# Performance work log

Hardware: AMD Instinct MI355X
Metric: run time of the kernel (lower is better)

The kernel has to match this reference:

```python
import jax, jax.numpy as jnp
import numpy as np

N_EMBD = 1024
HEAD_SIZE = N_EMBD  # source bug: Block passes n_embd as head_size
EPS = 1e-5

def layernorm(x, g, b):
    mu = jnp.mean(x, axis=-1, keepdims=True)
    var = jnp.var(x, axis=-1, keepdims=True)
    return (x - mu) * jax.lax.rsqrt(var + EPS) * g + b

def setup_inputs() -> dict:
    key = jax.random.key(0)
    ks = jax.random.split(key, 8)
    B, T, C = 4, 2048, N_EMBD
    s = lambda fan_in: 1.0 / np.sqrt(fan_in)
    return {
        "x": jax.random.normal(ks[0], (B, T, C), dtype=jnp.float32),
        "Wk": jax.random.uniform(ks[1], (C, HEAD_SIZE), jnp.float32, -s(C), s(C)),
        "Wq": jax.random.uniform(ks[2], (C, HEAD_SIZE), jnp.float32, -s(C), s(C)),
        "Wv": jax.random.uniform(ks[3], (C, HEAD_SIZE), jnp.float32, -s(C), s(C)),
        "W1": jax.random.uniform(ks[4], (C, 4 * C), jnp.float32, -s(C), s(C)),
        "b1": jnp.zeros((4 * C,), jnp.float32),
        "W2": jax.random.uniform(ks[5], (4 * C, C), jnp.float32, -s(4 * C), s(4 * C)),
        "b2": jnp.zeros((C,), jnp.float32),
        "g1": jnp.ones((C,), jnp.float32),
        "be1": jnp.zeros((C,), jnp.float32),
        "g2": jnp.ones((C,), jnp.float32),
        "be2": jnp.zeros((C,), jnp.float32),
    }

def reference(x, Wk, Wq, Wv, W1, b1, W2, b2, g1, be1, g2, be2):
    B, T, C = x.shape
    h = layernorm(x, g1, be1)
    q = h @ Wq              # [B,T,H]
    k = h @ Wk
    v = h @ Wv
    wei = jnp.einsum('bth,bsh->bts', q, k) / jnp.sqrt(jnp.float32(C))
    causal = jnp.tril(jnp.ones((T, T), dtype=bool))
    wei = jnp.where(causal, wei, -jnp.inf)
    wei = jax.nn.softmax(wei, axis=-1)
    sa = jnp.einsum('bts,bsh->bth', wei, v)
    x = x + sa
    h2 = layernorm(x, g2, be2)
    ff = jax.nn.relu(h2 @ W1 + b1) @ W2 + b2
    return x + ff
```

## Files before the change

kernel.cpp:

```cpp
#include <hip/hip_runtime.h>
#include <hip/hip_bf16.h>


typedef __bf16 bf16x8_t __attribute__((ext_vector_type(8)));
typedef float f32x4_t __attribute__((ext_vector_type(4)));

__device__ __forceinline__ unsigned short f2bf(float f) {
    unsigned int u = __float_as_uint(f);
    u += 0x7fffu + ((u >> 16) & 1u);
    return (unsigned short)(u >> 16);
}
__device__ __forceinline__ float bf2f(unsigned short u) {
    return __uint_as_float((unsigned int)u << 16);
}

__device__ __forceinline__ void gload16(const void* g, void* lds) {
    __builtin_amdgcn_global_load_lds(
        (const __attribute__((address_space(1))) unsigned int*)g,
        (__attribute__((address_space(3))) unsigned int*)lds, 16, 0, 0);
}

#define SB0() __builtin_amdgcn_sched_barrier(0)
#define BAR_LGKM() asm volatile("s_barrier\ns_waitcnt lgkmcnt(0)" ::: "memory")
#define BAR() asm volatile("s_barrier" ::: "memory")
#define VM4_BAR() asm volatile("s_waitcnt vmcnt(4)\ns_barrier" ::: "memory")
#define VM0_BAR() asm volatile("s_waitcnt vmcnt(0)\ns_barrier" ::: "memory")

enum { EPI_F32 = 0, EPI_BF16 = 1, EPI_BIAS_RELU_BF16 = 2, EPI_RESID_F32 = 3,
       EPI_BIAS_RESID_F32 = 4 };

template <int EPI, bool CSKIP, bool KLIM>
__global__ __launch_bounds__(512, 2) void gemm256(
    const unsigned short* __restrict__ A,
    const unsigned short* __restrict__ Bm,
    void* __restrict__ Cout,
    const float* __restrict__ bias,
    const float* __restrict__ resid,
    int M, int N, int K, int lda, int ldb, float scale,
    long long batA, long long batB, long long batC, long long batR)
{
    __shared__ __align__(16) unsigned char lds[131072];

    const int gx = gridDim.x;
    const int nwg = gx * gridDim.y;
    int bl = blockIdx.y * gx + blockIdx.x;
    bl = (bl & 7) * (nwg >> 3) + (bl >> 3);
    const int bx = bl % gx, by = bl / gx;

    const int row0 = by * 256, col0 = bx * 256;
    if (CSKIP && col0 > row0) return;

    const int bz = blockIdx.z;
    const unsigned short* Ab = A + (long long)bz * batA + (long long)row0 * lda;
    const unsigned short* Bb = Bm + (long long)bz * batB + (long long)col0 * ldb;

    const int tid = threadIdx.x, lane = tid & 63, wid = tid >> 6;
    const int wrM = (wid >> 2) * 128;
    const int wcN = (wid & 3) * 64;
    const int lr = lane & 15, lg = lane >> 4;

    int Keff = K;
    if (KLIM) { int kl = row0 + 256; Keff = kl < K ? kl : K; }
    const int nkt = Keff >> 6;

    const int c0 = wid * 128 + lane;
    const int crow = c0 >> 2;
    const int sg = (c0 & 3) ^ ((c0 >> 3) & 3);
    const unsigned short* gA0 = Ab + (long long)crow * lda + sg * 8;
    const unsigned short* gA1 = gA0 + 16ll * lda;
    const unsigned short* gB0 = Bb + (long long)crow * ldb + sg * 8;
    const unsigned short* gB1 = gB0 + 16ll * ldb;

    const int sw = (lg ^ ((lr >> 1) & 3)) << 4;
    const int aoff = (wrM + lr) * 64 + sw;
    const int boff = 16384 + (wcN + lr) * 64 + sw;

    f32x4_t acc[8][4];
#pragma unroll
    for (int m = 0; m < 8; ++m)
#pragma unroll
        for (int n = 0; n < 4; ++n)
            acc[m][n] = (f32x4_t){0.f, 0.f, 0.f, 0.f};

    auto stageR = [&](int b, int r, int ktn) {
        const int kk = r >> 1, op = r & 1;
        const int ke = ktn * 64 + kk * 32;
        unsigned char* d = lds + b * 65536 + kk * 32768 + op * 16384 + wid * 2048;
        const unsigned short* g0 = (op ? gB0 : gA0) + ke;
        const unsigned short* g1 = (op ? gB1 : gA1) + ke;
        gload16(g0, d);
        gload16(g1, d + 1024);
    };

    bf16x8_t af[4], bv[4];
    auto dsA4 = [&](int b, int kk, int mq) {
        const unsigned char* u = lds + b * 65536 + kk * 32768;
#pragma unroll
        for (int j = 0; j < 4; ++j)
            af[j] = *(const bf16x8_t*)(u + aoff + (mq * 4 + j) * 1024);
    };
    auto dsB4 = [&](int b, int kk) {
        const unsigned char* u = lds + b * 65536 + kk * 32768;
#pragma unroll
        for (int n = 0; n < 4; ++n)
            bv[n] = *(const bf16x8_t*)(u + boff + n * 1024);
    };
    auto mf16 = [&](int mq) {
        __builtin_amdgcn_s_setprio(1);
#pragma unroll
        for (int j = 0; j < 4; ++j)
#pragma unroll
            for (int n = 0; n < 4; ++n)
                acc[mq * 4 + j][n] = __builtin_amdgcn_mfma_f32_16x16x32_bf16(
                    af[j], bv[n], acc[mq * 4 + j][n], 0, 0, 0);
        __builtin_amdgcn_s_setprio(0);
    };

    stageR(0, 0, 0); stageR(0, 1, 0); stageR(0, 2, 0); stageR(0, 3, 0);
    VM4_BAR();

    int kt = 0;
    for (; kt < nkt - 1; ++kt) {
        const int buf = kt & 1, nb = buf ^ 1;
        dsA4(buf, 0, 0); dsB4(buf, 0);
        stageR(nb, 0, kt + 1);
        BAR_LGKM(); SB0();
        mf16(0); SB0();
        BAR();
        dsA4(buf, 0, 1);
        stageR(nb, 1, kt + 1);
        BAR_LGKM(); SB0();
        mf16(1); SB0();
        VM4_BAR();
        dsA4(buf, 1, 0); dsB4(buf, 1);
        stageR(nb, 2, kt + 1);
        BAR_LGKM(); SB0();
        mf16(0); SB0();
        BAR();
        dsA4(buf, 1, 1);
        stageR(nb, 3, kt + 1);
        BAR_LGKM(); SB0();
        mf16(1); SB0();
        VM4_BAR();
    }
    {
        const int buf = kt & 1;
        dsA4(buf, 0, 0); dsB4(buf, 0);
        BAR_LGKM(); SB0();
        mf16(0); SB0();
        BAR();
        dsA4(buf, 0, 1);
        BAR_LGKM(); SB0();
        mf16(1); SB0();
        VM0_BAR();
        dsA4(buf, 1, 0); dsB4(buf, 1);
        BAR_LGKM(); SB0();
        mf16(0); SB0();
        BAR();
        dsA4(buf, 1, 1);
        BAR_LGKM(); SB0();
        mf16(1); SB0();
    }

    const int ldc = N;
    float* Cf = (float*)Cout + (long long)bz * batC;
    unsigned short* Cb = (unsigned short*)Cout + (long long)bz * batC;
    const float* R = nullptr;
    if constexpr (EPI == EPI_RESID_F32 || EPI == EPI_BIAS_RESID_F32)
        R = resid + (long long)bz * batR;

#pragma unroll
    for (int m = 0; m < 8; ++m)
#pragma unroll
        for (int n = 0; n < 4; ++n)
#pragma unroll
            for (int j = 0; j < 4; ++j) {
                const int row = row0 + wrM + m * 16 + lg * 4 + j;
                const int col = col0 + wcN + n * 16 + lr;
                const long long idx = (long long)row * ldc + col;
                float v = acc[m][n][j] * scale;
                if constexpr (EPI == EPI_F32) {
                    Cf[idx] = v;
                } else if constexpr (EPI == EPI_BF16) {
                    Cb[idx] = f2bf(v);
                } else if constexpr (EPI == EPI_BIAS_RELU_BF16) {
                    v += bias[col];
                    v = v > 0.f ? v : 0.f;
                    Cb[idx] = f2bf(v);
                } else if constexpr (EPI == EPI_RESID_F32) {
                    Cf[idx] = v + R[idx];
                } else {
                    Cf[idx] = v + bias[col] + R[idx];
                }
            }
}

template <int EPI, bool CSKIP, bool KLIM>
__global__ __launch_bounds__(256, 2) void gemm128(
    const unsigned short* __restrict__ A,
    const unsigned short* __restrict__ Bm,
    void* __restrict__ Cout,
    const float* __restrict__ bias,
    const float* __restrict__ resid,
    int M, int N, int K, int lda, int ldb, float scale,
    long long batA, long long batB, long long batC, long long batR)
{
    __shared__ __align__(16) unsigned char lds[65536];

    const int gx = gridDim.x;
    const int nwg = gx * gridDim.y;
    int bl = blockIdx.y * gx + blockIdx.x;
    bl = (bl & 7) * (nwg >> 3) + (bl >> 3);
    const int bx = bl % gx, by = bl / gx;

    const int row0 = by * 128, col0 = bx * 128;
    if (CSKIP && col0 > row0) return;

    const int bz = blockIdx.z;
    const unsigned short* Ab = A + (long long)bz * batA + (long long)row0 * lda;
    const unsigned short* Bb = Bm + (long long)bz * batB + (long long)col0 * ldb;

    const int tid = threadIdx.x, lane = tid & 63, wid = tid >> 6;
    const int wrM = (wid >> 1) * 64;
    const int wcN = (wid & 1) * 64;
    const int lr = lane & 15, lg = lane >> 4;

    int Keff = K;
    if (KLIM) { int kl = row0 + 128; Keff = kl < K ? kl : K; }
    const int nkt = Keff >> 6;

    const int c0 = wid * 128 + lane;
    const int crow = c0 >> 2;
    const int sg = (c0 & 3) ^ ((c0 >> 3) & 3);
    const unsigned short* gA0 = Ab + (long long)crow * lda + sg * 8;
    const unsigned short* gA1 = gA0 + 16ll * lda;
    const unsigned short* gB0 = Bb + (long long)crow * ldb + sg * 8;
    const unsigned short* gB1 = gB0 + 16ll * ldb;

    const int sw = (lg ^ ((lr >> 1) & 3)) << 4;
    const int aoff = (wrM + lr) * 64 + sw;
    const int boff = 8192 + (wcN + lr) * 64 + sw;

    f32x4_t acc[4][4];
#pragma unroll
    for (int m = 0; m < 4; ++m)
#pragma unroll
        for (int n = 0; n < 4; ++n)
            acc[m][n] = (f32x4_t){0.f, 0.f, 0.f, 0.f};

    auto stage2 = [&](int b, int kk, int ktn) {
        const int ke = ktn * 64 + kk * 32;
        unsigned char* uA = lds + b * 32768 + kk * 16384 + wid * 2048;
        unsigned char* uB = uA + 8192;
        gload16(gA0 + ke, uA);
        gload16(gA1 + ke, uA + 1024);
        gload16(gB0 + ke, uB);
        gload16(gB1 + ke, uB + 1024);
    };

    bf16x8_t af[4], bv[4];
    auto dsAB = [&](int b, int kk) {
        const unsigned char* u = lds + b * 32768 + kk * 16384;
#pragma unroll
        for (int m = 0; m < 4; ++m)
            af[m] = *(const bf16x8_t*)(u + aoff + m * 1024);
#pragma unroll
        for (int n = 0; n < 4; ++n)
            bv[n] = *(const bf16x8_t*)(u + boff + n * 1024);
    };
    auto mf16 = [&]() {
        __builtin_amdgcn_s_setprio(1);
#pragma unroll
        for (int m = 0; m < 4; ++m)
#pragma unroll
            for (int n = 0; n < 4; ++n)
                acc[m][n] = __builtin_amdgcn_mfma_f32_16x16x32_bf16(
                    af[m], bv[n], acc[m][n], 0, 0, 0);
        __builtin_amdgcn_s_setprio(0);
    };

    stage2(0, 0, 0); stage2(0, 1, 0);
    VM4_BAR();

    int kt = 0;
    for (; kt < nkt - 1; ++kt) {
        const int buf = kt & 1, nb = buf ^ 1;
        dsAB(buf, 0);
        stage2(nb, 0, kt + 1);
        BAR_LGKM(); SB0();
        mf16(); SB0();
        VM4_BAR();
        dsAB(buf, 1);
        stage2(nb, 1, kt + 1);
        BAR_LGKM(); SB0();
        mf16(); SB0();
        VM4_BAR();
    }
    {
        const int buf = kt & 1;
        dsAB(buf, 0);
        BAR_LGKM(); SB0();
        mf16(); SB0();
        VM0_BAR();
        dsAB(buf, 1);
        BAR_LGKM(); SB0();
        mf16(); SB0();
    }

    const int ldc = N;
    float* Cf = (float*)Cout + (long long)bz * batC;
    unsigned short* Cb = (unsigned short*)Cout + (long long)bz * batC;
    const float* R = nullptr;
    if constexpr (EPI == EPI_RESID_F32 || EPI == EPI_BIAS_RESID_F32)
        R = resid + (long long)bz * batR;

#pragma unroll
    for (int m = 0; m < 4; ++m)
#pragma unroll
        for (int n = 0; n < 4; ++n)
#pragma unroll
            for (int j = 0; j < 4; ++j) {
                const int row = row0 + wrM + m * 16 + lg * 4 + j;
                const int col = col0 + wcN + n * 16 + lr;
                const long long idx = (long long)row * ldc + col;
                float v = acc[m][n][j] * scale;
                if constexpr (EPI == EPI_F32) {
                    Cf[idx] = v;
                } else if constexpr (EPI == EPI_BF16) {
                    Cb[idx] = f2bf(v);
                } else if constexpr (EPI == EPI_BIAS_RELU_BF16) {
                    v += bias[col];
                    v = v > 0.f ? v : 0.f;
                    Cb[idx] = f2bf(v);
                } else if constexpr (EPI == EPI_RESID_F32) {
                    Cf[idx] = v + R[idx];
                } else {
                    Cf[idx] = v + bias[col] + R[idx];
                }
            }
}

__global__ __launch_bounds__(256, 2) void pv_k(
    const unsigned short* __restrict__ Pm,
    const unsigned short* __restrict__ vT,
    float* __restrict__ xres,
    const float* __restrict__ x,
    int Tt, int Cc, int BT)
{
    __shared__ __align__(16) unsigned char lds[65536];

    const int gx = gridDim.x;
    const int nwg = gx * gridDim.y;
    int bl = blockIdx.y * gx + blockIdx.x;
    bl = (bl & 7) * (nwg >> 3) + (bl >> 3);
    const int bx = bl % gx, by = bl / gx;
    const int bz = blockIdx.z;

    const int col0 = bx * 128;
    const int tid = threadIdx.x, lane = tid & 63, wid = tid >> 6;
    const int wrM = (wid >> 1) * 64;
    const int wcN = (wid & 1) * 64;
    const int lr = lane & 15, lg = lane >> 4;

    const int c0 = wid * 128 + lane;
    const int crow = c0 >> 2;
    const int sg = (c0 & 3) ^ ((c0 >> 3) & 3);

    const int lda = Tt, ldb = BT, ldc = Cc;
    const unsigned short* Bb = vT + (long long)bz * Tt + (long long)col0 * ldb;
    const unsigned short* gB0 = Bb + (long long)crow * ldb + sg * 8;
    const unsigned short* gB1 = gB0 + 16ll * ldb;

    const int sw = (lg ^ ((lr >> 1) & 3)) << 4;
    const int aoff = (wrM + lr) * 64 + sw;
    const int boff = 8192 + (wcN + lr) * 64 + sw;

    bf16x8_t af[4], bv[4];
    auto dsAB = [&](int b, int kk) {
        const unsigned char* u = lds + b * 32768 + kk * 16384;
#pragma unroll
        for (int m = 0; m < 4; ++m)
            af[m] = *(const bf16x8_t*)(u + aoff + m * 1024);
#pragma unroll
        for (int n = 0; n < 4; ++n)
            bv[n] = *(const bf16x8_t*)(u + boff + n * 1024);
    };

    float* Cf = xres + (long long)bz * Tt * Cc;
    const float* R = x + (long long)bz * Tt * Cc;

    for (int pass = 0; pass < 2; ++pass) {
        const int by_eff = pass ? (15 - by) : by;
        const int row0 = by_eff * 128;
        const int nkt = (row0 + 128) >> 6;

        const unsigned short* Ab = Pm + (long long)bz * Tt * Tt + (long long)row0 * lda;
        const unsigned short* gA0 = Ab + (long long)crow * lda + sg * 8;
        const unsigned short* gA1 = gA0 + 16ll * lda;

        auto stage2 = [&](int b, int kk, int ktn) {
            const int ke = ktn * 64 + kk * 32;
            unsigned char* uA = lds + b * 32768 + kk * 16384 + wid * 2048;
            unsigned char* uB = uA + 8192;
            gload16(gA0 + ke, uA);
            gload16(gA1 + ke, uA + 1024);
            gload16(gB0 + ke, uB);
            gload16(gB1 + ke, uB + 1024);
        };

        f32x4_t acc[4][4];
#pragma unroll
        for (int m = 0; m < 4; ++m)
#pragma unroll
            for (int n = 0; n < 4; ++n)
                acc[m][n] = (f32x4_t){0.f, 0.f, 0.f, 0.f};

        auto mf16 = [&]() {
            __builtin_amdgcn_s_setprio(1);
#pragma unroll
            for (int m = 0; m < 4; ++m)
#pragma unroll
                for (int n = 0; n < 4; ++n)
                    acc[m][n] = __builtin_amdgcn_mfma_f32_16x16x32_bf16(
                        af[m], bv[n], acc[m][n], 0, 0, 0);
            __builtin_amdgcn_s_setprio(0);
        };

        if (pass) BAR();
        stage2(0, 0, 0); stage2(0, 1, 0);
        VM4_BAR();

        int kt = 0;
        for (; kt < nkt - 1; ++kt) {
            const int buf = kt & 1, nb = buf ^ 1;
            dsAB(buf, 0);
            stage2(nb, 0, kt + 1);
            BAR_LGKM(); SB0();
            mf16(); SB0();
            VM4_BAR();
            dsAB(buf, 1);
            stage2(nb, 1, kt + 1);
            BAR_LGKM(); SB0();
            mf16(); SB0();
            VM4_BAR();
        }
        {
            const int buf = kt & 1;
            dsAB(buf, 0);
            BAR_LGKM(); SB0();
            mf16(); SB0();
            VM0_BAR();
            dsAB(buf, 1);
            BAR_LGKM(); SB0();
            mf16(); SB0();
        }

#pragma unroll
        for (int m = 0; m < 4; ++m)
#pragma unroll
            for (int n = 0; n < 4; ++n)
#pragma unroll
                for (int j = 0; j < 4; ++j) {
                    const int row = row0 + wrM + m * 16 + lg * 4 + j;
                    const int col = col0 + wcN + n * 16 + lr;
                    const long long idx = (long long)row * ldc + col;
                    Cf[idx] = acc[m][n][j] + R[idx];
                }
    }
}

__global__ __launch_bounds__(256) void tconv_k(
    const float* __restrict__ in, unsigned short* __restrict__ out,
    int R, int Cc)
{
    __shared__ float t[64][65];
    const int r0 = blockIdx.y * 64, c0 = blockIdx.x * 64;
    const int tid = threadIdx.x;
    const int a = tid >> 4;
    const int b = tid & 15;
#pragma unroll
    for (int i = 0; i < 4; ++i) {
        const int row = a + i * 16;
        float4 v = *(const float4*)(in + (long long)(r0 + row) * Cc + c0 + b * 4);
        t[row][b * 4 + 0] = v.x; t[row][b * 4 + 1] = v.y;
        t[row][b * 4 + 2] = v.z; t[row][b * 4 + 3] = v.w;
    }
    __syncthreads();
#pragma unroll
    for (int i = 0; i < 4; ++i) {
        const int oc = a + i * 16;
        ushort4 o;
        o.x = f2bf(t[b * 4 + 0][oc]);
        o.y = f2bf(t[b * 4 + 1][oc]);
        o.z = f2bf(t[b * 4 + 2][oc]);
        o.w = f2bf(t[b * 4 + 3][oc]);
        *(ushort4*)(out + (long long)(c0 + oc) * R + r0 + b * 4) = o;
    }
}

__global__ __launch_bounds__(256) void vtrans_k(
    const unsigned short* __restrict__ in, unsigned short* __restrict__ out)
{
    __shared__ unsigned short t[64][72];
    const int r0 = blockIdx.x * 64;
    const int c0 = blockIdx.y * 64;
    const int tid = threadIdx.x;
#pragma unroll
    for (int i = 0; i < 2; ++i) {
        const int ch = tid * 2 + i;
        const int row = ch >> 3, cs = ch & 7;
        int4 v = *(const int4*)(in + (long long)(r0 + row) * 3072 + 2048 + c0 + cs * 8);
        *(int4*)&t[row][cs * 8] = v;
    }
    __syncthreads();
#pragma unroll
    for (int i = 0; i < 2; ++i) {
        const int w = tid * 2 + i;
        const int oc = w >> 3, orc = w & 7;
        unsigned short tmp[8];
#pragma unroll
        for (int j = 0; j < 8; ++j) tmp[j] = t[orc * 8 + j][oc];
        *(int4*)(out + (long long)(c0 + oc) * 8192 + r0 + orc * 8) = *(const int4*)tmp;
    }
}

__global__ __launch_bounds__(256) void ln_k(
    const float* __restrict__ x, const float* __restrict__ g,
    const float* __restrict__ be, unsigned short* __restrict__ out)
{
    const int wv = threadIdx.x >> 6, lane = threadIdx.x & 63;
    const long long row = blockIdx.x * 4 + wv;
    const float* xr = x + row * 1024;
    float4 v[4];
    float s = 0.f, q = 0.f;
#pragma unroll
    for (int j = 0; j < 4; ++j) {
        v[j] = *(const float4*)(xr + j * 256 + lane * 4);
        s += v[j].x + v[j].y + v[j].z + v[j].w;
        q += v[j].x * v[j].x + v[j].y * v[j].y + v[j].z * v[j].z + v[j].w * v[j].w;
    }
#pragma unroll
    for (int off = 32; off > 0; off >>= 1) {
        s += __shfl_xor(s, off);
        q += __shfl_xor(q, off);
    }
    const float mean = s * (1.0f / 1024.0f);
    const float var  = q * (1.0f / 1024.0f) - mean * mean;
    const float rstd = rsqrtf(var + 1e-5f);
#pragma unroll
    for (int j = 0; j < 4; ++j) {
        float4 gv = *(const float4*)(g + j * 256 + lane * 4);
        float4 bv = *(const float4*)(be + j * 256 + lane * 4);
        ushort4 o;
        o.x = f2bf((v[j].x - mean) * rstd * gv.x + bv.x);
        o.y = f2bf((v[j].y - mean) * rstd * gv.y + bv.y);
        o.z = f2bf((v[j].z - mean) * rstd * gv.z + bv.z);
        o.w = f2bf((v[j].w - mean) * rstd * gv.w + bv.w);
        *(ushort4*)(out + row * 1024 + j * 256 + lane * 4) = o;
    }
}

__global__ __launch_bounds__(256) void softmax_k(
    const unsigned short* __restrict__ S, unsigned short* __restrict__ P, int T)
{
    __shared__ float rowl[2048];
    __shared__ float sred[4];
    const int t = blockIdx.x;
    const long long base = ((long long)blockIdx.y * T + t) * (long long)T;
    const unsigned short* srow = S + base;
    unsigned short* prow = P + base;
    const int n = t + 1;
    const int lim = ((t >> 7) + 1) << 7;
    const int tid = threadIdx.x;

    const int n8 = n >> 3;
    for (int i = tid; i < n8; i += 256) {
        int4 r = ((const int4*)srow)[i];
        const unsigned short* u = (const unsigned short*)&r;
#pragma unroll
        for (int j = 0; j < 8; ++j) rowl[i * 8 + j] = bf2f(u[j]);
    }
    for (int i = (n8 << 3) + tid; i < n; i += 256) rowl[i] = bf2f(srow[i]);
    __syncthreads();

    float mx = -3.0e38f;
    for (int i = tid; i < n; i += 256) mx = fmaxf(mx, rowl[i]);
#pragma unroll
    for (int off = 32; off > 0; off >>= 1) mx = fmaxf(mx, __shfl_xor(mx, off));
    if ((tid & 63) == 0) sred[tid >> 6] = mx;
    __syncthreads();
    mx = fmaxf(fmaxf(sred[0], sred[1]), fmaxf(sred[2], sred[3]));
    __syncthreads();

    float sum = 0.f;
    for (int i = tid; i < n; i += 256) {
        float e = __expf(rowl[i] - mx);
        rowl[i] = e;
        sum += e;
    }
#pragma unroll
    for (int off = 32; off > 0; off >>= 1) sum += __shfl_xor(sum, off);
    if ((tid & 63) == 0) sred[tid >> 6] = sum;
    __syncthreads();
    sum = sred[0] + sred[1] + sred[2] + sred[3];
    const float inv = 1.0f / sum;

    for (int i = tid; i < n; i += 256) prow[i] = f2bf(rowl[i] * inv);
    for (int i = n + tid; i < lim; i += 256) prow[i] = 0;
}

extern "C" void kernel_launch(void* const* d_in, const int* in_sizes, int n_in,
                              void* d_out, int out_size, void* d_ws, size_t ws_size,
                              hipStream_t stream)
{
    const int B = 4, T = 2048, C = 1024, F = 4096;
    const float* x   = (const float*)d_in[0];
    const float* Wk  = (const float*)d_in[1];
    const float* Wq  = (const float*)d_in[2];
    const float* Wv  = (const float*)d_in[3];
    const float* W1  = (const float*)d_in[4];
    const float* b1  = (const float*)d_in[5];
    const float* W2  = (const float*)d_in[6];
    const float* b2  = (const float*)d_in[7];
    const float* g1  = (const float*)d_in[8];
    const float* be1 = (const float*)d_in[9];
    const float* g2  = (const float*)d_in[10];
    const float* be2 = (const float*)d_in[11];

    char* ws = (char*)d_ws;
    const size_t MB = 1ull << 20;
    unsigned short* h     = (unsigned short*)(ws + 0);
    unsigned short* qkv   = (unsigned short*)(ws + 16 * MB);
    unsigned short* vT    = (unsigned short*)(ws + 64 * MB);
    float*          xres  = (float*)(ws + 80 * MB);
    unsigned short* S     = (unsigned short*)(ws + 112 * MB);
    unsigned short* P     = (unsigned short*)(ws + 144 * MB);
    unsigned short* ff1   = (unsigned short*)(ws + 112 * MB);
    unsigned short* wqkvT = (unsigned short*)(ws + 176 * MB);
    unsigned short* w1T   = (unsigned short*)(ws + 182 * MB);
    unsigned short* w2T   = (unsigned short*)(ws + 190 * MB);

    tconv_k<<<dim3(16, 16), 256, 0, stream>>>(Wq, wqkvT, C, C);
    tconv_k<<<dim3(16, 16), 256, 0, stream>>>(Wk, wqkvT + C * C, C, C);
    tconv_k<<<dim3(16, 16), 256, 0, stream>>>(Wv, wqkvT + 2 * C * C, C, C);
    tconv_k<<<dim3(64, 16), 256, 0, stream>>>(W1, w1T, C, F);
    tconv_k<<<dim3(16, 64), 256, 0, stream>>>(W2, w2T, F, C);

    ln_k<<<dim3(B * T / 4), 256, 0, stream>>>(x, g1, be1, h);

    dim3 gqkv(3 * C / 256, (B * T) / 256, 1);
    gemm256<EPI_BF16, false, false><<<gqkv, 512, 0, stream>>>(
        h, wqkvT, qkv, nullptr, nullptr, B * T, 3 * C, C, C, C, 1.0f, 0, 0, 0, 0);

    vtrans_k<<<dim3(B * T / 64, C / 64), 256, 0, stream>>>(qkv, vT);

    dim3 gsc(T / 128, T / 128, B);
    gemm128<EPI_BF16, true, false><<<gsc, 256, 0, stream>>>(
        qkv, qkv + C, S, nullptr, nullptr, T, T, C, 3 * C, 3 * C, 0.03125f,
        (long long)T * 3 * C, (long long)T * 3 * C, (long long)T * T, 0);

    softmax_k<<<dim3(T, B), 256, 0, stream>>>(S, P, T);

    pv_k<<<dim3(C / 128, 8, B), 256, 0, stream>>>(
        P, vT, xres, x, T, C, B * T);

    ln_k<<<dim3(B * T / 4), 256, 0, stream>>>(xres, g2, be2, h);

    dim3 gf1(F / 256, (B * T) / 256, 1);
    gemm256<EPI_BIAS_RELU_BF16, false, false><<<gf1, 512, 0, stream>>>(
        h, w1T, ff1, b1, nullptr, B * T, F, C, C, C, 1.0f, 0, 0, 0, 0);

    dim3 gf2(C / 128, (B * T) / 128, 1);
    gemm128<EPI_BIAS_RESID_F32, false, false><<<gf2, 256, 0, stream>>>(
        ff1, w2T, (float*)d_out, b2, xres, B * T, C, F, F, F, 1.0f, 0, 0, 0, 0);
}
```

Measured before the change: 372.6 us.

## Use one wavefront per softmax row and 256-tile GEMM for attention scores

The softmax kernel now handles four rows per block, one per wavefront. Each row is kept in registers with 16-byte vector loads and stores, which removes the shared-memory staging and block-wide barriers. Masked tail elements are written as zero inside the same vector store, so the separate zero-fill loop is gone. The QK^T score GEMM switches from the 128-tile kernel to the 256-tile kernel with 512 threads, aiming for more data reuse. In exchange, register pressure rises (32 floats per lane), and the causal score GEMM may have poorer tail balance with fewer, larger tiles.

```diff
diff --git a/kernel.cpp b/kernel.cpp
--- a/kernel.cpp
+++ b/kernel.cpp
@@ -563,50 +563,61 @@
 __global__ __launch_bounds__(256) void softmax_k(
     const unsigned short* __restrict__ S, unsigned short* __restrict__ P, int T)
 {
-    __shared__ float rowl[2048];
-    __shared__ float sred[4];
-    const int t = blockIdx.x;
+    const int wv = threadIdx.x >> 6, lane = threadIdx.x & 63;
+    const int t = blockIdx.x * 4 + wv;
     const long long base = ((long long)blockIdx.y * T + t) * (long long)T;
     const unsigned short* srow = S + base;
     unsigned short* prow = P + base;
     const int n = t + 1;
     const int lim = ((t >> 7) + 1) << 7;
-    const int tid = threadIdx.x;
-
-    const int n8 = n >> 3;
-    for (int i = tid; i < n8; i += 256) {
-        int4 r = ((const int4*)srow)[i];
-        const unsigned short* u = (const unsigned short*)&r;
-#pragma unroll
-        for (int j = 0; j < 8; ++j) rowl[i * 8 + j] = bf2f(u[j]);
-    }
-    for (int i = (n8 << 3) + tid; i < n; i += 256) rowl[i] = bf2f(srow[i]);
-    __syncthreads();
-
+    const int nch = (lim + 511) >> 9;
+
+    float v[4][8];
     float mx = -3.0e38f;
-    for (int i = tid; i < n; i += 256) mx = fmaxf(mx, rowl[i]);
+#pragma unroll
+    for (int j = 0; j < 4; ++j) {
+        if (j < nch) {
+            const int e0 = (j * 64 + lane) * 8;
+            int4 r = *(const int4*)(srow + e0);
+            const unsigned short* u = (const unsigned short*)&r;
+#pragma unroll
+            for (int i = 0; i < 8; ++i) {
+                float f = bf2f(u[i]);
+                v[j][i] = f;
+                if (e0 + i < n) mx = fmaxf(mx, f);
+            }
+        }
+    }
 #pragma unroll
     for (int off = 32; off > 0; off >>= 1) mx = fmaxf(mx, __shfl_xor(mx, off));
-    if ((tid & 63) == 0) sred[tid >> 6] = mx;
-    __syncthreads();
-    mx = fmaxf(fmaxf(sred[0], sred[1]), fmaxf(sred[2], sred[3]));
-    __syncthreads();
 
     float sum = 0.f;
-    for (int i = tid; i < n; i += 256) {
-        float e = __expf(rowl[i] - mx);
-        rowl[i] = e;
-        sum += e;
+#pragma unroll
+    for (int j = 0; j < 4; ++j) {
+        if (j < nch) {
+            const int e0 = (j * 64 + lane) * 8;
+#pragma unroll
+            for (int i = 0; i < 8; ++i) {
+                float e = (e0 + i < n) ? __expf(v[j][i] - mx) : 0.f;
+                v[j][i] = e;
+                sum += e;
+            }
+        }
     }
 #pragma unroll
     for (int off = 32; off > 0; off >>= 1) sum += __shfl_xor(sum, off);
-    if ((tid & 63) == 0) sred[tid >> 6] = sum;
-    __syncthreads();
-    sum = sred[0] + sred[1] + sred[2] + sred[3];
     const float inv = 1.0f / sum;
 
-    for (int i = tid; i < n; i += 256) prow[i] = f2bf(rowl[i] * inv);
-    for (int i = n + tid; i < lim; i += 256) prow[i] = 0;
+#pragma unroll
+    for (int j = 0; j < 4; ++j) {
+        if (j < nch) {
+            const int e0 = (j * 64 + lane) * 8;
+            unsigned short o[8];
+#pragma unroll
+            for (int i = 0; i < 8; ++i) o[i] = f2bf(v[j][i] * inv);
+            *(int4*)(prow + e0) = *(const int4*)o;
+        }
+    }
 }
 
 extern "C" void kernel_launch(void* const* d_in, const int* in_sizes, int n_in,
@@ -654,12 +665,12 @@
 
     vtrans_k<<<dim3(B * T / 64, C / 64), 256, 0, stream>>>(qkv, vT);
 
-    dim3 gsc(T / 128, T / 128, B);
-    gemm128<EPI_BF16, true, false><<<gsc, 256, 0, stream>>>(
+    dim3 gsc(T / 256, T / 256, B);
+    gemm256<EPI_BF16, true, false><<<gsc, 512, 0, stream>>>(
         qkv, qkv + C, S, nullptr, nullptr, T, T, C, 3 * C, 3 * C, 0.03125f,
         (long long)T * 3 * C, (long long)T * 3 * C, (long long)T * T, 0);
 
-    softmax_k<<<dim3(T, B), 256, 0, stream>>>(S, P, T);
+    softmax_k<<<dim3(T / 4, B), 256, 0, stream>>>(S, P, T);
 
     pv_k<<<dim3(C / 128, 8, B), 256, 0, stream>>>(
         P, vT, xres, x, T, C, B * T);
```

Result: faster. 358.1 us (-3.9%).
